# Kernel tuning notes

Hardware: AMD Instinct MI355X
Metric: run time of the kernel (lower is better)

The kernel has to match this reference:

```python
import jax, jax.numpy as jnp
import numpy as np

T, B, N = 1000, 64, 512
DT = 0.01
EL, VR, TR, TINF = -0.07, -0.07, -0.06, -0.05
A_VAL = 2.6239240169525146
A1_VAL = -0.015625353902578354
A2_VAL = -1.0590057373046875
B_VAL = 12.77495288848877
G_VAL = 45.24007797241211
K1, K2 = 200.0, 20.0
R1, R2 = 0.3858567178249359, -1.1421641111373901
C = 1.0


def setup_inputs() -> dict:
    key = jax.random.key(0)
    x = jax.random.normal(key, (T, B, N), dtype=jnp.float32)
    linear = jnp.ones((1, N), jnp.float32)
    a = jnp.full((1, N), A_VAL, jnp.float32)
    A1 = jnp.full((1, N), A1_VAL * C, jnp.float32)
    A2 = jnp.full((1, N), A2_VAL * C, jnp.float32)
    return {"x": x, "linear": linear, "a": a, "A1": A1, "A2": A2}


def _spike(v):
    # Heaviside step (forward of SurrGradSpike)
    return (v > 0).astype(v.dtype)


def reference(x, linear, a, A1, A2):
    G = G_VAL * C

    def step(state, xt):
        V, i1, i2, Thr = state
        i1 = i1 - K1 * i1 * DT
        i2 = i2 - K2 * i2 * DT
        V = V + DT * (linear * xt + i1 + i2 - G * (V - EL)) / C
        Thr = Thr + DT * (a * (V - EL) - B_VAL * (Thr - TINF))
        spk = _spike(V - Thr)
        i1 = (1.0 - spk) * i1 + spk * (R1 * i1 + A1)
        i2 = (1.0 - spk) * i2 + spk * (R2 * i2 + A2)
        Thr = (1.0 - spk) * Thr + spk * jnp.maximum(Thr, TR)
        V = (1.0 - spk) * V + spk * VR
        return (V, i1, i2, Thr), spk

    Bd, Nd = x.shape[1], x.shape[2]
    init = (
        jnp.full((Bd, Nd), EL, x.dtype),   # V
        jnp.zeros((Bd, Nd), x.dtype),      # i1
        jnp.zeros((Bd, Nd), x.dtype),      # i2
        jnp.full((Bd, Nd), TINF, x.dtype), # Thr
    )
    _, spikes = jax.lax.scan(step, init, x)
    return spikes  # [T, B, N] (original returns np.array of per-step spikes)
```

## Files before the change

kernel.cpp:

```cpp
#include <hip/hip_runtime.h>


#define T_STEPS 1000
#define B_DIM 64
#define N_DIM 512
#define BN (B_DIM * N_DIM)

#define K_CHUNK 20
#define NCHUNK (T_STEPS / K_CHUNK)
#define NBUF 4

#define C_DT   0.01f
#define C_EL   (-0.07f)
#define C_VR   (-0.07f)
#define C_TR   (-0.06f)
#define C_TINF (-0.05f)
#define C_B    12.77495288848877f
#define C_G    45.24007797241211f
#define C_K1   200.0f
#define C_K2   20.0f
#define C_R1   0.3858567178249359f
#define C_R2   (-1.1421641111373901f)

typedef const __attribute__((address_space(1))) void* gp_t;
typedef __attribute__((address_space(3))) void* lp_t;

__device__ __forceinline__ void raw_barrier() {
    asm volatile("s_barrier" ::: "memory");
}

__device__ __forceinline__ float mn_step(float xt, float lin, float av,
                                         float A1v, float A2v,
                                         float& V, float& i1, float& i2,
                                         float& Thr)
{
#pragma clang fp contract(off)
    i1 = i1 - (C_K1 * i1) * C_DT;
    i2 = i2 - (C_K2 * i2) * C_DT;
    float p  = lin * xt;
    float q  = p + i1;
    float r  = q + i2;
    float e  = V - C_EL;
    float g  = C_G * e;
    float s  = r - g;
    float d  = C_DT * s;
    V = V + d;
    float e2 = V - C_EL;
    float u  = av * e2;
    float w  = Thr - C_TINF;
    float bw = C_B * w;
    float s2 = u - bw;
    float d2 = C_DT * s2;
    Thr = Thr + d2;
    float diff = V - Thr;
    bool  sb   = diff > 0.0f;
    float spk  = sb ? 1.0f : 0.0f;
    float i1r = (C_R1 * i1) + A1v;
    float i2r = (C_R2 * i2) + A2v;
    i1  = sb ? i1r : i1;
    i2  = sb ? i2r : i2;
    float tm = fmaxf(Thr, C_TR);
    Thr = sb ? tm : Thr;
    V   = sb ? C_VR : V;
    return spk;
}

__global__ __launch_bounds__(128) void mn_neuron_kernel(
    const float* __restrict__ x, const float* __restrict__ linear,
    const float* __restrict__ a, const float* __restrict__ A1,
    const float* __restrict__ A2, float* __restrict__ out)
{
#pragma clang fp contract(off)
    __shared__ float lds[NBUF][K_CHUNK][64];

    const int lane = threadIdx.x & 63;
    const int wid  = threadIdx.x >> 6;
    const int blk  = blockIdx.x;

    if (wid == 1) {
        const float* pl = x + (size_t)(lane >> 4) * BN
                            + (size_t)blk * 64 + (size_t)(lane & 15) * 4;

        auto issue = [&](int k) {
            const float* pc = pl + (size_t)(k * K_CHUNK) * BN;
            float* dst = &lds[k & (NBUF - 1)][0][0];
#pragma unroll
            for (int s = 0; s < K_CHUNK / 4; ++s) {
                __builtin_amdgcn_global_load_lds(
                    (gp_t)(pc + (size_t)(s * 4) * BN),
                    (lp_t)(dst + s * 4 * 64), 16, 0, 0);
            }
        };

        issue(0); issue(1); issue(2);
        asm volatile("s_waitcnt vmcnt(10)" ::: "memory");
        raw_barrier();

        for (int c = 0; c < NCHUNK - 3; ++c) {
            issue(c + 3);
            asm volatile("s_waitcnt vmcnt(10)" ::: "memory");
            raw_barrier();
        }
        asm volatile("s_waitcnt vmcnt(5)" ::: "memory");
        raw_barrier();
        asm volatile("s_waitcnt vmcnt(0)" ::: "memory");
        raw_barrier();
        raw_barrier();
    } else {
        const int idx = blk * 64 + lane;
        const int n   = idx & (N_DIM - 1);

        const float lin = linear[n];
        const float av  = a[n];
        const float A1v = A1[n];
        const float A2v = A2[n];

        float V   = C_EL;
        float i1  = 0.0f;
        float i2  = 0.0f;
        float Thr = C_TINF;

        float* op = out + idx;

        raw_barrier();

        for (int c = 0; c < NCHUNK; ++c) {
            const float* src = &lds[c & (NBUF - 1)][0][lane];

            float xv[K_CHUNK];
#pragma unroll
            for (int j = 0; j < K_CHUNK; ++j)
                xv[j] = src[j * 64];
#pragma unroll
            for (int j = 0; j < K_CHUNK; ++j)
                asm volatile("" : "+v"(xv[j]));

#pragma unroll
            for (int j = 0; j < K_CHUNK; ++j) {
                float spk = mn_step(xv[j], lin, av, A1v, A2v, V, i1, i2, Thr);
                __builtin_nontemporal_store(spk, op);
                op += BN;
            }
            raw_barrier();
        }
    }
}

extern "C" void kernel_launch(void* const* d_in, const int* in_sizes, int n_in,
                              void* d_out, int out_size, void* d_ws, size_t ws_size,
                              hipStream_t stream) {
    const float* x      = (const float*)d_in[0];
    const float* linear = (const float*)d_in[1];
    const float* a      = (const float*)d_in[2];
    const float* A1     = (const float*)d_in[3];
    const float* A2     = (const float*)d_in[4];
    float* out = (float*)d_out;

    mn_neuron_kernel<<<BN / 64, 128, 0, stream>>>(x, linear, a, A1, A2, out);
}
```

Before: 236.5 us.

## Merge producer and consumer waves, process two neurons per lane with packed math

Removes the dedicated loader wave and its s_barrier handshakes. A single 64-thread wave now issues its own global-to-LDS prefetches and computes two neurons per lane using float2 vector arithmetic, which can map to packed FP32 instructions. Each block covers 128 neurons, so the grid is half as many blocks with half as many threads each. This trades barrier and cross-wave synchronisation for lower wave count. Synchronisation now relies on vmcnt waits, which also count the nontemporal stores and may stall more than intended.

```diff
diff --git a/kernel.cpp b/kernel.cpp
--- a/kernel.cpp
+++ b/kernel.cpp
@@ -9,6 +9,7 @@
 #define K_CHUNK 20
 #define NCHUNK (T_STEPS / K_CHUNK)
 #define NBUF 4
+#define CPB 128
 
 #define C_DT   0.01f
 #define C_EL   (-0.07f)
@@ -24,124 +25,121 @@
 
 typedef const __attribute__((address_space(1))) void* gp_t;
 typedef __attribute__((address_space(3))) void* lp_t;
+typedef float v2f __attribute__((ext_vector_type(2)));
 
-__device__ __forceinline__ void raw_barrier() {
-    asm volatile("s_barrier" ::: "memory");
-}
-
-__device__ __forceinline__ float mn_step(float xt, float lin, float av,
-                                         float A1v, float A2v,
-                                         float& V, float& i1, float& i2,
-                                         float& Thr)
+__device__ __forceinline__ v2f mn_step2(v2f xt, v2f lin, v2f av,
+                                        v2f A1v, v2f A2v,
+                                        v2f& V, v2f& i1, v2f& i2, v2f& Thr)
 {
 #pragma clang fp contract(off)
     i1 = i1 - (C_K1 * i1) * C_DT;
     i2 = i2 - (C_K2 * i2) * C_DT;
-    float p  = lin * xt;
-    float q  = p + i1;
-    float r  = q + i2;
-    float e  = V - C_EL;
-    float g  = C_G * e;
-    float s  = r - g;
-    float d  = C_DT * s;
+    v2f p  = lin * xt;
+    v2f q  = p + i1;
+    v2f r  = q + i2;
+    v2f e  = V - C_EL;
+    v2f g  = C_G * e;
+    v2f s  = r - g;
+    v2f d  = C_DT * s;
     V = V + d;
-    float e2 = V - C_EL;
-    float u  = av * e2;
-    float w  = Thr - C_TINF;
-    float bw = C_B * w;
-    float s2 = u - bw;
-    float d2 = C_DT * s2;
+    v2f e2 = V - C_EL;
+    v2f u  = av * e2;
+    v2f w  = Thr - C_TINF;
+    v2f bw = C_B * w;
+    v2f s2 = u - bw;
+    v2f d2 = C_DT * s2;
     Thr = Thr + d2;
-    float diff = V - Thr;
-    bool  sb   = diff > 0.0f;
-    float spk  = sb ? 1.0f : 0.0f;
-    float i1r = (C_R1 * i1) + A1v;
-    float i2r = (C_R2 * i2) + A2v;
-    i1  = sb ? i1r : i1;
-    i2  = sb ? i2r : i2;
-    float tm = fmaxf(Thr, C_TR);
-    Thr = sb ? tm : Thr;
-    V   = sb ? C_VR : V;
+    v2f diff = V - Thr;
+    v2f i1r = (C_R1 * i1) + A1v;
+    v2f i2r = (C_R2 * i2) + A2v;
+
+    v2f spk;
+    {
+        bool sb = diff.x > 0.0f;
+        spk.x = sb ? 1.0f : 0.0f;
+        i1.x  = sb ? i1r.x : i1.x;
+        i2.x  = sb ? i2r.x : i2.x;
+        float tm = fmaxf(Thr.x, C_TR);
+        Thr.x = sb ? tm : Thr.x;
+        V.x   = sb ? C_VR : V.x;
+    }
+    {
+        bool sb = diff.y > 0.0f;
+        spk.y = sb ? 1.0f : 0.0f;
+        i1.y  = sb ? i1r.y : i1.y;
+        i2.y  = sb ? i2r.y : i2.y;
+        float tm = fmaxf(Thr.y, C_TR);
+        Thr.y = sb ? tm : Thr.y;
+        V.y   = sb ? C_VR : V.y;
+    }
     return spk;
 }
 
-__global__ __launch_bounds__(128) void mn_neuron_kernel(
+__global__ __launch_bounds__(64) void mn_neuron_kernel(
     const float* __restrict__ x, const float* __restrict__ linear,
     const float* __restrict__ a, const float* __restrict__ A1,
     const float* __restrict__ A2, float* __restrict__ out)
 {
 #pragma clang fp contract(off)
-    __shared__ float lds[NBUF][K_CHUNK][64];
+    __shared__ float lds[NBUF][K_CHUNK][CPB];
 
-    const int lane = threadIdx.x & 63;
-    const int wid  = threadIdx.x >> 6;
+    const int lane = threadIdx.x;
     const int blk  = blockIdx.x;
+    const int base = blk * CPB;
+    const int idx0 = base + lane;
+    const int idx1 = idx0 + 64;
 
-    if (wid == 1) {
-        const float* pl = x + (size_t)(lane >> 4) * BN
-                            + (size_t)blk * 64 + (size_t)(lane & 15) * 4;
+    const float* pl = x + (size_t)base + (size_t)(lane >> 5) * BN
+                        + (size_t)(lane & 31) * 4;
 
-        auto issue = [&](int k) {
-            const float* pc = pl + (size_t)(k * K_CHUNK) * BN;
-            float* dst = &lds[k & (NBUF - 1)][0][0];
+    auto issue = [&](int k) {
+        const float* pc = pl + (size_t)(k * K_CHUNK) * BN;
+        float* dst = &lds[k & (NBUF - 1)][0][0];
 #pragma unroll
-            for (int s = 0; s < K_CHUNK / 4; ++s) {
-                __builtin_amdgcn_global_load_lds(
-                    (gp_t)(pc + (size_t)(s * 4) * BN),
-                    (lp_t)(dst + s * 4 * 64), 16, 0, 0);
-            }
-        };
+        for (int s = 0; s < K_CHUNK / 2; ++s) {
+            __builtin_amdgcn_global_load_lds(
+                (gp_t)(pc + (size_t)(2 * s) * BN),
+                (lp_t)(dst + 2 * s * CPB), 16, 0, 0);
+        }
+    };
 
-        issue(0); issue(1); issue(2);
-        asm volatile("s_waitcnt vmcnt(10)" ::: "memory");
-        raw_barrier();
+    issue(0); issue(1); issue(2);
 
-        for (int c = 0; c < NCHUNK - 3; ++c) {
-            issue(c + 3);
-            asm volatile("s_waitcnt vmcnt(10)" ::: "memory");
-            raw_barrier();
-        }
-        asm volatile("s_waitcnt vmcnt(5)" ::: "memory");
-        raw_barrier();
-        asm volatile("s_waitcnt vmcnt(0)" ::: "memory");
-        raw_barrier();
-        raw_barrier();
-    } else {
-        const int idx = blk * 64 + lane;
-        const int n   = idx & (N_DIM - 1);
+    const int n0 = idx0 & (N_DIM - 1);
+    const int n1 = idx1 & (N_DIM - 1);
+    v2f lin = {linear[n0], linear[n1]};
+    v2f av  = {a[n0],      a[n1]};
+    v2f A1v = {A1[n0],     A1[n1]};
+    v2f A2v = {A2[n0],     A2[n1]};
 
-        const float lin = linear[n];
-        const float av  = a[n];
-        const float A1v = A1[n];
-        const float A2v = A2[n];
+    v2f V   = {C_EL,   C_EL};
+    v2f i1  = {0.0f,   0.0f};
+    v2f i2  = {0.0f,   0.0f};
+    v2f Thr = {C_TINF, C_TINF};
 
-        float V   = C_EL;
-        float i1  = 0.0f;
-        float i2  = 0.0f;
-        float Thr = C_TINF;
+    float* op = out + idx0;
 
-        float* op = out + idx;
+    asm volatile("s_waitcnt vmcnt(20)" ::: "memory");
 
-        raw_barrier();
-
-        for (int c = 0; c < NCHUNK; ++c) {
-            const float* src = &lds[c & (NBUF - 1)][0][lane];
-
-            float xv[K_CHUNK];
-#pragma unroll
-            for (int j = 0; j < K_CHUNK; ++j)
-                xv[j] = src[j * 64];
-#pragma unroll
-            for (int j = 0; j < K_CHUNK; ++j)
-                asm volatile("" : "+v"(xv[j]));
+    for (int c = 0; c < NCHUNK; ++c) {
+        const float* src = &lds[c & (NBUF - 1)][0][lane];
 
 #pragma unroll
-            for (int j = 0; j < K_CHUNK; ++j) {
-                float spk = mn_step(xv[j], lin, av, A1v, A2v, V, i1, i2, Thr);
-                __builtin_nontemporal_store(spk, op);
-                op += BN;
-            }
-            raw_barrier();
+        for (int j = 0; j < K_CHUNK; ++j) {
+            v2f xt = {src[j * CPB], src[j * CPB + 64]};
+            v2f spk = mn_step2(xt, lin, av, A1v, A2v, V, i1, i2, Thr);
+            __builtin_nontemporal_store(spk.x, op);
+            __builtin_nontemporal_store(spk.y, op + 64);
+            op += BN;
+        }
+
+        if (c + 3 < NCHUNK) {
+            issue(c + 3);
+            asm volatile("s_waitcnt vmcnt(20)" ::: "memory");
+        } else if (c == NCHUNK - 3) {
+            asm volatile("s_waitcnt vmcnt(10)" ::: "memory");
+        } else if (c == NCHUNK - 2) {
+            asm volatile("s_waitcnt vmcnt(0)" ::: "memory");
         }
     }
 }
@@ -156,5 +154,5 @@
     const float* A2     = (const float*)d_in[4];
     float* out = (float*)d_out;
 
-    mn_neuron_kernel<<<BN / 64, 128, 0, stream>>>(x, linear, a, A1, A2, out);
+    mn_neuron_kernel<<<BN / CPB, 64, 0, stream>>>(x, linear, a, A1, A2, out);
 }
```

New measurement: 272.9 us. 1.15x slower.
